# Kernel optimization log

Measured on AMD Instinct MI355X. Metric: run time of the kernel, lower is better.

Reference implementation:

```python
import jax, jax.numpy as jnp
import numpy as np

N_NODES = 100000
N_EDGES = 3200000  # avg degree 32
D_IN = 128
D_OUT = 64
BN_EPS = 0.001


def setup_inputs() -> dict:
    key = jax.random.key(0)
    k1, k2, k3, k4, k5 = jax.random.split(key, 5)
    x = jax.random.normal(k1, (N_NODES, D_IN), dtype=jnp.float32)
    W = jax.random.normal(k2, (D_IN, D_OUT), dtype=jnp.float32) * 0.05
    edge_val = jax.random.uniform(k3, (N_EDGES,), dtype=jnp.float32)
    edge_src = jax.random.randint(k4, (N_EDGES,), 0, N_NODES, dtype=jnp.int32)
    edge_dst = jax.random.randint(k5, (N_EDGES,), 0, N_NODES, dtype=jnp.int32)
    return {"x": x, "W": W, "edge_val": edge_val,
            "edge_src": edge_src, "edge_dst": edge_dst}


def reference(x, W, edge_val, edge_src, edge_dst):
    # pre_sup = X @ W  (dense feature transform; dropout rate is 0 -> identity)
    pre_sup = x @ W  # [N, D_OUT]
    # support = A @ pre_sup, A given in COO form: A[dst, src] = edge_val
    msgs = edge_val[:, None] * pre_sup[edge_src]          # [E, D_OUT]
    out = jax.ops.segment_sum(msgs, edge_dst, num_segments=N_NODES)  # [N, D_OUT]
    # tf.nn.moments over all-but-last axis + batch_norm (no scale/offset, eps=1e-3)
    mean = jnp.mean(out, axis=0)
    var = jnp.var(out, axis=0)
    out = (out - mean) * jax.lax.rsqrt(var + BN_EPS)
    return jax.nn.relu(out)
```

## Files before the change

kernel.cpp:

```cpp
#include <hip/hip_runtime.h>
#include <stdint.h>

#define D_IN  128
#define D_OUT 64
#define BN_EPS 1e-3f

#define BIN_SHIFT 6
#define BIN_NODES 64
#define BIN_CAP   2560
#define CHUNK     8192
#define MAX_BINS  1600
#define PT_STRIDE 72

typedef __attribute__((ext_vector_type(8))) short bf16x8;
typedef __attribute__((ext_vector_type(4))) float f32x4;

__device__ __forceinline__ ushort f32_to_bf16_rne(float f) {
  uint u = __float_as_uint(f);
  u += 0x7FFFu + ((u >> 16) & 1u);
  return (ushort)(u >> 16);
}
__device__ __forceinline__ float bf16_to_f32(ushort h) {
  return __uint_as_float((uint)h << 16);
}

__global__ __launch_bounds__(256) void gemm_mfma_kernel(
    const float* __restrict__ x, const float* __restrict__ W,
    ushort* __restrict__ pre16, int* __restrict__ bin_cursor,
    float* __restrict__ stats, int n_bins, int n_nodes, int n_tiles) {
  __shared__ ushort Wb[D_IN * D_OUT];
  __shared__ ushort ptile[64 * PT_STRIDE];
  const int t = threadIdx.x;
  if (blockIdx.x == 0) {
    for (int i = t; i < n_bins; i += 256) bin_cursor[i] = 0;
    if (t < 128) stats[t] = 0.f;
  }
  for (int i = t; i < D_IN * D_OUT; i += 256) Wb[i] = f32_to_bf16_rne(W[i]);
  __syncthreads();

  const int lane = t & 63;
  const int wave = t >> 6;
  const int m = lane & 15;
  const int quad = lane >> 4;

  bf16x8 bfrag[4][4];
#pragma unroll
  for (int nt = 0; nt < 4; ++nt)
#pragma unroll
    for (int s = 0; s < 4; ++s)
#pragma unroll
      for (int j = 0; j < 8; ++j)
        bfrag[nt][s][j] =
            (short)Wb[(32 * s + quad * 8 + j) * D_OUT + nt * 16 + m];

  for (int tile = blockIdx.x; tile < n_tiles; tile += gridDim.x) {
    const int rbase0 = tile * 64;
    const int row = rbase0 + wave * 16 + m;
    const size_t rl = (size_t)min(row, n_nodes - 1);
    f32x4 acc0 = {0.f, 0.f, 0.f, 0.f}, acc1 = {0.f, 0.f, 0.f, 0.f};
    f32x4 acc2 = {0.f, 0.f, 0.f, 0.f}, acc3 = {0.f, 0.f, 0.f, 0.f};
#pragma unroll
    for (int s = 0; s < 4; ++s) {
      const float4 xa = *(const float4*)&x[rl * D_IN + s * 32 + quad * 8];
      const float4 xb = *(const float4*)&x[rl * D_IN + s * 32 + quad * 8 + 4];
      bf16x8 af;
      af[0] = (short)f32_to_bf16_rne(xa.x);
      af[1] = (short)f32_to_bf16_rne(xa.y);
      af[2] = (short)f32_to_bf16_rne(xa.z);
      af[3] = (short)f32_to_bf16_rne(xa.w);
      af[4] = (short)f32_to_bf16_rne(xb.x);
      af[5] = (short)f32_to_bf16_rne(xb.y);
      af[6] = (short)f32_to_bf16_rne(xb.z);
      af[7] = (short)f32_to_bf16_rne(xb.w);
      acc0 = __builtin_amdgcn_mfma_f32_16x16x32_bf16(af, bfrag[0][s], acc0, 0, 0, 0);
      acc1 = __builtin_amdgcn_mfma_f32_16x16x32_bf16(af, bfrag[1][s], acc1, 0, 0, 0);
      acc2 = __builtin_amdgcn_mfma_f32_16x16x32_bf16(af, bfrag[2][s], acc2, 0, 0, 0);
      acc3 = __builtin_amdgcn_mfma_f32_16x16x32_bf16(af, bfrag[3][s], acc3, 0, 0, 0);
    }
    __syncthreads();
#pragma unroll
    for (int reg = 0; reg < 4; ++reg) {
      const int lr = wave * 16 + quad * 4 + reg;
      ptile[lr * PT_STRIDE + m]      = f32_to_bf16_rne(acc0[reg]);
      ptile[lr * PT_STRIDE + 16 + m] = f32_to_bf16_rne(acc1[reg]);
      ptile[lr * PT_STRIDE + 32 + m] = f32_to_bf16_rne(acc2[reg]);
      ptile[lr * PT_STRIDE + 48 + m] = f32_to_bf16_rne(acc3[reg]);
    }
    __syncthreads();
    {
      const int lr = t >> 2;
      const int sg = t & 3;
      const int r = rbase0 + lr;
      if (r < n_nodes) {
        const uint4* pl = (const uint4*)&ptile[lr * PT_STRIDE + sg * 16];
        uint4* po = (uint4*)&pre16[(size_t)r * D_OUT + sg * 16];
        po[0] = pl[0];
        po[1] = pl[1];
      }
    }
  }
}

__global__ __launch_bounds__(256) void partition_kernel(
    const float* __restrict__ ev, const int* __restrict__ esrc,
    const int* __restrict__ edst, int* __restrict__ bin_cursor,
    uint2* __restrict__ bucket, int n_edges, int n_bins) {
  __shared__ int cnt[MAX_BINS];
  __shared__ int base[MAX_BINS];
  const int t = threadIdx.x;
  const int beg = blockIdx.x * CHUNK;
  const int end = min(beg + CHUNK, n_edges);

  for (int i = t; i < n_bins; i += 256) cnt[i] = 0;
  __syncthreads();

  for (int i = beg + t * 4; i < end; i += 1024) {
    if (i + 3 < end) {
      const int4 d4 = *(const int4*)&edst[i];
      atomicAdd(&cnt[d4.x >> BIN_SHIFT], 1);
      atomicAdd(&cnt[d4.y >> BIN_SHIFT], 1);
      atomicAdd(&cnt[d4.z >> BIN_SHIFT], 1);
      atomicAdd(&cnt[d4.w >> BIN_SHIFT], 1);
    } else {
      for (int k = i; k < end; ++k) atomicAdd(&cnt[edst[k] >> BIN_SHIFT], 1);
    }
  }
  __syncthreads();

  for (int i = t; i < n_bins; i += 256) {
    const int c = cnt[i];
    int b = 0;
    if (c > 0) b = atomicAdd(&bin_cursor[i], c);
    if (b > BIN_CAP) b = BIN_CAP;
    base[i] = i * BIN_CAP + b;
    cnt[i] = 0;
  }
  __syncthreads();

  for (int i = beg + t * 4; i < end; i += 1024) {
    if (i + 3 < end) {
      const int4 d4 = *(const int4*)&edst[i];
      const int4 s4 = *(const int4*)&esrc[i];
      const float4 v4 = *(const float4*)&ev[i];
#pragma unroll
      for (int k = 0; k < 4; ++k) {
        const int dst = (&d4.x)[k];
        const int src = (&s4.x)[k];
        const float v = (&v4.x)[k];
        const int bin = dst >> BIN_SHIFT;
        const int r = atomicAdd(&cnt[bin], 1);
        const int pos = base[bin] + r;
        if (pos < (bin + 1) * BIN_CAP) {
          const uint w0 = ((uint)(dst & (BIN_NODES - 1)) << 17) | (uint)src;
          bucket[pos] = make_uint2(w0, __float_as_uint(v));
        }
      }
    } else {
      for (int k = i; k < end; ++k) {
        const int dst = edst[k];
        const int bin = dst >> BIN_SHIFT;
        const int r = atomicAdd(&cnt[bin], 1);
        const int pos = base[bin] + r;
        if (pos < (bin + 1) * BIN_CAP) {
          const uint w0 = ((uint)(dst & (BIN_NODES - 1)) << 17) | (uint)esrc[k];
          bucket[pos] = make_uint2(w0, __float_as_uint(ev[k]));
        }
      }
    }
  }
}

__global__ __launch_bounds__(512) void bin_sort_gather_kernel(
    const ushort* __restrict__ pre16, const uint2* __restrict__ bucket,
    const int* __restrict__ bin_cursor, float* __restrict__ out,
    float* __restrict__ stats, int n_nodes) {
  __shared__ uint s_src[BIN_CAP];
  __shared__ ushort s_val[BIN_CAP];
  __shared__ int s_hist[BIN_NODES];
  __shared__ int s_off[BIN_NODES + 1];
  __shared__ int s_cur[BIN_NODES];

  const int t = threadIdx.x;
  const int bin = blockIdx.x;
  const int cnt = min(bin_cursor[bin], BIN_CAP);
  const int64_t rbase = (int64_t)bin * BIN_CAP;

  if (t < BIN_NODES) s_hist[t] = 0;
  __syncthreads();

  for (int i = t; i < cnt; i += 512)
    atomicAdd(&s_hist[bucket[rbase + i].x >> 17], 1);
  __syncthreads();

  int own = (t < BIN_NODES) ? s_hist[t] : 0;
  for (int off = 1; off < BIN_NODES; off <<= 1) {
    int u = 0;
    if (t < BIN_NODES && t >= off) u = s_hist[t - off];
    __syncthreads();
    if (t < BIN_NODES) s_hist[t] += u;
    __syncthreads();
  }
  if (t < BIN_NODES) {
    const int e = s_hist[t] - own;
    s_off[t] = e;
    s_cur[t] = e;
  }
  if (t == 0) s_off[BIN_NODES] = cnt;
  __syncthreads();

  for (int i = t; i < cnt; i += 512) {
    const uint2 r = bucket[rbase + i];
    const int d = r.x >> 17;
    const int p = atomicAdd(&s_cur[d], 1);
    s_src[p] = r.x & 0x1FFFFu;
    s_val[p] = f32_to_bf16_rne(__uint_as_float(r.y));
  }
  __syncthreads();

  const int lane = t & 63;
  const int wave = t >> 6;
  const int half = lane >> 5;
  const int hl = lane & 31;
  const int node0 = bin * BIN_NODES;
  float csx = 0.f, csy = 0.f, cs2x = 0.f, cs2y = 0.f;

  for (int nl = wave; nl < BIN_NODES; nl += 8) {
    const int node = node0 + nl;
    if (node < n_nodes) {
      const int jb = s_off[nl], je = s_off[nl + 1];
      float a0x = 0.f, a0y = 0.f, a1x = 0.f, a1y = 0.f;
      float a2x = 0.f, a2y = 0.f, a3x = 0.f, a3y = 0.f;
      float a4x = 0.f, a4y = 0.f, a5x = 0.f, a5y = 0.f;
      float a6x = 0.f, a6y = 0.f, a7x = 0.f, a7y = 0.f;
      int j = jb + half;
      for (; j + 14 < je; j += 16) {
        const uint src0 = s_src[j],      src1 = s_src[j + 2];
        const uint src2 = s_src[j + 4],  src3 = s_src[j + 6];
        const uint src4 = s_src[j + 8],  src5 = s_src[j + 10];
        const uint src6 = s_src[j + 12], src7 = s_src[j + 14];
        const float v0 = bf16_to_f32(s_val[j]);
        const float v1 = bf16_to_f32(s_val[j + 2]);
        const float v2 = bf16_to_f32(s_val[j + 4]);
        const float v3 = bf16_to_f32(s_val[j + 6]);
        const float v4 = bf16_to_f32(s_val[j + 8]);
        const float v5 = bf16_to_f32(s_val[j + 10]);
        const float v6 = bf16_to_f32(s_val[j + 12]);
        const float v7 = bf16_to_f32(s_val[j + 14]);
        const uint p0 = *(const uint*)&pre16[(size_t)src0 * D_OUT + 2 * hl];
        const uint p1 = *(const uint*)&pre16[(size_t)src1 * D_OUT + 2 * hl];
        const uint p2 = *(const uint*)&pre16[(size_t)src2 * D_OUT + 2 * hl];
        const uint p3 = *(const uint*)&pre16[(size_t)src3 * D_OUT + 2 * hl];
        const uint p4 = *(const uint*)&pre16[(size_t)src4 * D_OUT + 2 * hl];
        const uint p5 = *(const uint*)&pre16[(size_t)src5 * D_OUT + 2 * hl];
        const uint p6 = *(const uint*)&pre16[(size_t)src6 * D_OUT + 2 * hl];
        const uint p7 = *(const uint*)&pre16[(size_t)src7 * D_OUT + 2 * hl];
        a0x += v0 * bf16_to_f32((ushort)(p0 & 0xFFFFu));
        a0y += v0 * bf16_to_f32((ushort)(p0 >> 16));
        a1x += v1 * bf16_to_f32((ushort)(p1 & 0xFFFFu));
        a1y += v1 * bf16_to_f32((ushort)(p1 >> 16));
        a2x += v2 * bf16_to_f32((ushort)(p2 & 0xFFFFu));
        a2y += v2 * bf16_to_f32((ushort)(p2 >> 16));
        a3x += v3 * bf16_to_f32((ushort)(p3 & 0xFFFFu));
        a3y += v3 * bf16_to_f32((ushort)(p3 >> 16));
        a4x += v4 * bf16_to_f32((ushort)(p4 & 0xFFFFu));
        a4y += v4 * bf16_to_f32((ushort)(p4 >> 16));
        a5x += v5 * bf16_to_f32((ushort)(p5 & 0xFFFFu));
        a5y += v5 * bf16_to_f32((ushort)(p5 >> 16));
        a6x += v6 * bf16_to_f32((ushort)(p6 & 0xFFFFu));
        a6y += v6 * bf16_to_f32((ushort)(p6 >> 16));
        a7x += v7 * bf16_to_f32((ushort)(p7 & 0xFFFFu));
        a7y += v7 * bf16_to_f32((ushort)(p7 >> 16));
      }
      for (; j + 6 < je; j += 8) {
        const uint src0 = s_src[j],     src1 = s_src[j + 2];
        const uint src2 = s_src[j + 4], src3 = s_src[j + 6];
        const float v0 = bf16_to_f32(s_val[j]);
        const float v1 = bf16_to_f32(s_val[j + 2]);
        const float v2 = bf16_to_f32(s_val[j + 4]);
        const float v3 = bf16_to_f32(s_val[j + 6]);
        const uint p0 = *(const uint*)&pre16[(size_t)src0 * D_OUT + 2 * hl];
        const uint p1 = *(const uint*)&pre16[(size_t)src1 * D_OUT + 2 * hl];
        const uint p2 = *(const uint*)&pre16[(size_t)src2 * D_OUT + 2 * hl];
        const uint p3 = *(const uint*)&pre16[(size_t)src3 * D_OUT + 2 * hl];
        a0x += v0 * bf16_to_f32((ushort)(p0 & 0xFFFFu));
        a0y += v0 * bf16_to_f32((ushort)(p0 >> 16));
        a1x += v1 * bf16_to_f32((ushort)(p1 & 0xFFFFu));
        a1y += v1 * bf16_to_f32((ushort)(p1 >> 16));
        a2x += v2 * bf16_to_f32((ushort)(p2 & 0xFFFFu));
        a2y += v2 * bf16_to_f32((ushort)(p2 >> 16));
        a3x += v3 * bf16_to_f32((ushort)(p3 & 0xFFFFu));
        a3y += v3 * bf16_to_f32((ushort)(p3 >> 16));
      }
      for (; j < je; j += 2) {
        const uint src = s_src[j];
        const float v = bf16_to_f32(s_val[j]);
        const uint p = *(const uint*)&pre16[(size_t)src * D_OUT + 2 * hl];
        a0x += v * bf16_to_f32((ushort)(p & 0xFFFFu));
        a0y += v * bf16_to_f32((ushort)(p >> 16));
      }
      float ax = ((a0x + a1x) + (a2x + a3x)) + ((a4x + a5x) + (a6x + a7x));
      float ay = ((a0y + a1y) + (a2y + a3y)) + ((a4y + a5y) + (a6y + a7y));
      ax += __shfl_xor(ax, 32);
      ay += __shfl_xor(ay, 32);
      if (half == 0) {
        *(float2*)&out[(size_t)node * D_OUT + 2 * hl] = make_float2(ax, ay);
        csx += ax;
        cs2x += ax * ax;
        csy += ay;
        cs2y += ay * ay;
      }
    }
  }
  __syncthreads();

  float* red = (float*)s_src;
  float* red2 = red + 512;
  if (half == 0) {
    red[wave * 64 + 2 * hl] = csx;
    red[wave * 64 + 2 * hl + 1] = csy;
    red2[wave * 64 + 2 * hl] = cs2x;
    red2[wave * 64 + 2 * hl + 1] = cs2y;
  }
  __syncthreads();
  if (t < 64) {
    float s = 0.f, s2 = 0.f;
#pragma unroll
    for (int wv = 0; wv < 8; ++wv) {
      s += red[wv * 64 + t];
      s2 += red2[wv * 64 + t];
    }
    atomicAdd(&stats[t], s);
    atomicAdd(&stats[64 + t], s2);
  }
}

__global__ __launch_bounds__(256) void norm_kernel(
    float* __restrict__ out, const float* __restrict__ stats, int64_t n_vec4,
    float inv_n) {
  const int c = (threadIdx.x * 4) & 63;
  float mean[4], scale[4];
#pragma unroll
  for (int k = 0; k < 4; ++k) {
    mean[k] = stats[c + k] * inv_n;
    const float var = stats[64 + c + k] * inv_n - mean[k] * mean[k];
    scale[k] = rsqrtf(var + BN_EPS);
  }
  const int64_t stride = (int64_t)gridDim.x * 256;
  for (int64_t i = (int64_t)blockIdx.x * 256 + threadIdx.x; i < n_vec4;
       i += stride) {
    float4 v = ((float4*)out)[i];
    v.x = (v.x - mean[0]) * scale[0];
    v.y = (v.y - mean[1]) * scale[1];
    v.z = (v.z - mean[2]) * scale[2];
    v.w = (v.w - mean[3]) * scale[3];
    v.x = v.x > 0.f ? v.x : 0.f;
    v.y = v.y > 0.f ? v.y : 0.f;
    v.z = v.z > 0.f ? v.z : 0.f;
    v.w = v.w > 0.f ? v.w : 0.f;
    ((float4*)out)[i] = v;
  }
}

extern "C" void kernel_launch(void* const* d_in, const int* in_sizes, int n_in,
                              void* d_out, int out_size, void* d_ws,
                              size_t ws_size, hipStream_t stream) {
  const float* x = (const float*)d_in[0];
  const float* W = (const float*)d_in[1];
  const float* ev = (const float*)d_in[2];
  const int* esrc = (const int*)d_in[3];
  const int* edst = (const int*)d_in[4];

  const int n_nodes = in_sizes[0] / D_IN;
  const int n_edges = in_sizes[2];
  const int64_t n_out = (int64_t)n_nodes * D_OUT;
  const int n_bins = (n_nodes + BIN_NODES - 1) >> BIN_SHIFT;
  const int n_row_tiles = (n_nodes + 63) / 64;

  float* out = (float*)d_out;

  char* w = (char*)d_ws;
  ushort* pre16 = (ushort*)w;             w += (size_t)n_nodes * D_OUT * 2;
  int* bin_cursor = (int*)w;              w += (size_t)n_bins * 4;
  float* stats = (float*)w;               w += 128 * 4;
  w = (char*)(((uintptr_t)w + 7) & ~(uintptr_t)7);
  uint2* bucket = (uint2*)w;

  gemm_mfma_kernel<<<(n_row_tiles + 1) / 2, 256, 0, stream>>>(
      x, W, pre16, bin_cursor, stats, n_bins, n_nodes, n_row_tiles);
  partition_kernel<<<(n_edges + CHUNK - 1) / CHUNK, 256, 0, stream>>>(
      ev, esrc, edst, bin_cursor, bucket, n_edges, n_bins);
  bin_sort_gather_kernel<<<n_bins, 512, 0, stream>>>(pre16, bucket, bin_cursor,
                                                     out, stats, n_nodes);
  norm_kernel<<<2048, 256, 0, stream>>>(out, stats, n_out / 4,
                                        1.0f / (float)n_nodes);
}
```

Baseline: 299.3 us.

## Merge GEMM and edge partition into one launch with role-split blocks

Combines the dense MFMA GEMM and the edge-binning partition kernel into a single launch, where the first n_gemm blocks do the feature transform and the remaining blocks partition edges. The two independent phases can then run concurrently on the GPU and one launch gap disappears. Zeroing of the bin cursors and stats moves from GEMM block 0 into a hipMemsetAsync, which removes the ordering dependency that would otherwise make partitioning race with the reset. The shared memory becomes a union sized for the larger role, and the memset adds a small extra stream operation.

```diff
diff --git a/kernel.cpp b/kernel.cpp
--- a/kernel.cpp
+++ b/kernel.cpp
@@ -24,146 +24,143 @@
   return __uint_as_float((uint)h << 16);
 }
 
-__global__ __launch_bounds__(256) void gemm_mfma_kernel(
+__global__ __launch_bounds__(256) void gemm_partition_kernel(
     const float* __restrict__ x, const float* __restrict__ W,
-    ushort* __restrict__ pre16, int* __restrict__ bin_cursor,
-    float* __restrict__ stats, int n_bins, int n_nodes, int n_tiles) {
-  __shared__ ushort Wb[D_IN * D_OUT];
-  __shared__ ushort ptile[64 * PT_STRIDE];
+    const float* __restrict__ ev, const int* __restrict__ esrc,
+    const int* __restrict__ edst, ushort* __restrict__ pre16,
+    int* __restrict__ bin_cursor, uint2* __restrict__ bucket,
+    int n_nodes, int n_tiles, int n_edges, int n_bins, int n_gemm) {
+  __shared__ char smem[25600];
   const int t = threadIdx.x;
-  if (blockIdx.x == 0) {
-    for (int i = t; i < n_bins; i += 256) bin_cursor[i] = 0;
-    if (t < 128) stats[t] = 0.f;
-  }
-  for (int i = t; i < D_IN * D_OUT; i += 256) Wb[i] = f32_to_bf16_rne(W[i]);
-  __syncthreads();
-
-  const int lane = t & 63;
-  const int wave = t >> 6;
-  const int m = lane & 15;
-  const int quad = lane >> 4;
-
-  bf16x8 bfrag[4][4];
-#pragma unroll
-  for (int nt = 0; nt < 4; ++nt)
-#pragma unroll
-    for (int s = 0; s < 4; ++s)
-#pragma unroll
-      for (int j = 0; j < 8; ++j)
-        bfrag[nt][s][j] =
-            (short)Wb[(32 * s + quad * 8 + j) * D_OUT + nt * 16 + m];
-
-  for (int tile = blockIdx.x; tile < n_tiles; tile += gridDim.x) {
-    const int rbase0 = tile * 64;
-    const int row = rbase0 + wave * 16 + m;
-    const size_t rl = (size_t)min(row, n_nodes - 1);
-    f32x4 acc0 = {0.f, 0.f, 0.f, 0.f}, acc1 = {0.f, 0.f, 0.f, 0.f};
-    f32x4 acc2 = {0.f, 0.f, 0.f, 0.f}, acc3 = {0.f, 0.f, 0.f, 0.f};
-#pragma unroll
-    for (int s = 0; s < 4; ++s) {
-      const float4 xa = *(const float4*)&x[rl * D_IN + s * 32 + quad * 8];
-      const float4 xb = *(const float4*)&x[rl * D_IN + s * 32 + quad * 8 + 4];
-      bf16x8 af;
-      af[0] = (short)f32_to_bf16_rne(xa.x);
-      af[1] = (short)f32_to_bf16_rne(xa.y);
-      af[2] = (short)f32_to_bf16_rne(xa.z);
-      af[3] = (short)f32_to_bf16_rne(xa.w);
-      af[4] = (short)f32_to_bf16_rne(xb.x);
-      af[5] = (short)f32_to_bf16_rne(xb.y);
-      af[6] = (short)f32_to_bf16_rne(xb.z);
-      af[7] = (short)f32_to_bf16_rne(xb.w);
-      acc0 = __builtin_amdgcn_mfma_f32_16x16x32_bf16(af, bfrag[0][s], acc0, 0, 0, 0);
-      acc1 = __builtin_amdgcn_mfma_f32_16x16x32_bf16(af, bfrag[1][s], acc1, 0, 0, 0);
-      acc2 = __builtin_amdgcn_mfma_f32_16x16x32_bf16(af, bfrag[2][s], acc2, 0, 0, 0);
-      acc3 = __builtin_amdgcn_mfma_f32_16x16x32_bf16(af, bfrag[3][s], acc3, 0, 0, 0);
-    }
-    __syncthreads();
-#pragma unroll
-    for (int reg = 0; reg < 4; ++reg) {
-      const int lr = wave * 16 + quad * 4 + reg;
-      ptile[lr * PT_STRIDE + m]      = f32_to_bf16_rne(acc0[reg]);
-      ptile[lr * PT_STRIDE + 16 + m] = f32_to_bf16_rne(acc1[reg]);
-      ptile[lr * PT_STRIDE + 32 + m] = f32_to_bf16_rne(acc2[reg]);
-      ptile[lr * PT_STRIDE + 48 + m] = f32_to_bf16_rne(acc3[reg]);
-    }
-    __syncthreads();
-    {
-      const int lr = t >> 2;
-      const int sg = t & 3;
-      const int r = rbase0 + lr;
-      if (r < n_nodes) {
-        const uint4* pl = (const uint4*)&ptile[lr * PT_STRIDE + sg * 16];
-        uint4* po = (uint4*)&pre16[(size_t)r * D_OUT + sg * 16];
-        po[0] = pl[0];
-        po[1] = pl[1];
-      }
-    }
-  }
-}
-
-__global__ __launch_bounds__(256) void partition_kernel(
-    const float* __restrict__ ev, const int* __restrict__ esrc,
-    const int* __restrict__ edst, int* __restrict__ bin_cursor,
-    uint2* __restrict__ bucket, int n_edges, int n_bins) {
-  __shared__ int cnt[MAX_BINS];
-  __shared__ int base[MAX_BINS];
-  const int t = threadIdx.x;
-  const int beg = blockIdx.x * CHUNK;
-  const int end = min(beg + CHUNK, n_edges);
-
-  for (int i = t; i < n_bins; i += 256) cnt[i] = 0;
-  __syncthreads();
-
-  for (int i = beg + t * 4; i < end; i += 1024) {
-    if (i + 3 < end) {
-      const int4 d4 = *(const int4*)&edst[i];
-      atomicAdd(&cnt[d4.x >> BIN_SHIFT], 1);
-      atomicAdd(&cnt[d4.y >> BIN_SHIFT], 1);
-      atomicAdd(&cnt[d4.z >> BIN_SHIFT], 1);
-      atomicAdd(&cnt[d4.w >> BIN_SHIFT], 1);
-    } else {
-      for (int k = i; k < end; ++k) atomicAdd(&cnt[edst[k] >> BIN_SHIFT], 1);
-    }
-  }
-  __syncthreads();
-
-  for (int i = t; i < n_bins; i += 256) {
-    const int c = cnt[i];
-    int b = 0;
-    if (c > 0) b = atomicAdd(&bin_cursor[i], c);
-    if (b > BIN_CAP) b = BIN_CAP;
-    base[i] = i * BIN_CAP + b;
-    cnt[i] = 0;
-  }
-  __syncthreads();
-
-  for (int i = beg + t * 4; i < end; i += 1024) {
-    if (i + 3 < end) {
-      const int4 d4 = *(const int4*)&edst[i];
-      const int4 s4 = *(const int4*)&esrc[i];
-      const float4 v4 = *(const float4*)&ev[i];
-#pragma unroll
-      for (int k = 0; k < 4; ++k) {
-        const int dst = (&d4.x)[k];
-        const int src = (&s4.x)[k];
-        const float v = (&v4.x)[k];
-        const int bin = dst >> BIN_SHIFT;
-        const int r = atomicAdd(&cnt[bin], 1);
-        const int pos = base[bin] + r;
-        if (pos < (bin + 1) * BIN_CAP) {
-          const uint w0 = ((uint)(dst & (BIN_NODES - 1)) << 17) | (uint)src;
-          bucket[pos] = make_uint2(w0, __float_as_uint(v));
+
+  if ((int)blockIdx.x < n_gemm) {
+    ushort* Wb = (ushort*)smem;
+    ushort* ptile = (ushort*)(smem + 16384);
+    for (int i = t; i < D_IN * D_OUT; i += 256) Wb[i] = f32_to_bf16_rne(W[i]);
+    __syncthreads();
+
+    const int lane = t & 63;
+    const int wave = t >> 6;
+    const int m = lane & 15;
+    const int quad = lane >> 4;
+
+    bf16x8 bfrag[4][4];
+#pragma unroll
+    for (int nt = 0; nt < 4; ++nt)
+#pragma unroll
+      for (int s = 0; s < 4; ++s)
+#pragma unroll
+        for (int j = 0; j < 8; ++j)
+          bfrag[nt][s][j] =
+              (short)Wb[(32 * s + quad * 8 + j) * D_OUT + nt * 16 + m];
+
+    for (int tile = blockIdx.x; tile < n_tiles; tile += n_gemm) {
+      const int rbase0 = tile * 64;
+      const int row = rbase0 + wave * 16 + m;
+      const size_t rl = (size_t)min(row, n_nodes - 1);
+      f32x4 acc0 = {0.f, 0.f, 0.f, 0.f}, acc1 = {0.f, 0.f, 0.f, 0.f};
+      f32x4 acc2 = {0.f, 0.f, 0.f, 0.f}, acc3 = {0.f, 0.f, 0.f, 0.f};
+#pragma unroll
+      for (int s = 0; s < 4; ++s) {
+        const float4 xa = *(const float4*)&x[rl * D_IN + s * 32 + quad * 8];
+        const float4 xb = *(const float4*)&x[rl * D_IN + s * 32 + quad * 8 + 4];
+        bf16x8 af;
+        af[0] = (short)f32_to_bf16_rne(xa.x);
+        af[1] = (short)f32_to_bf16_rne(xa.y);
+        af[2] = (short)f32_to_bf16_rne(xa.z);
+        af[3] = (short)f32_to_bf16_rne(xa.w);
+        af[4] = (short)f32_to_bf16_rne(xb.x);
+        af[5] = (short)f32_to_bf16_rne(xb.y);
+        af[6] = (short)f32_to_bf16_rne(xb.z);
+        af[7] = (short)f32_to_bf16_rne(xb.w);
+        acc0 = __builtin_amdgcn_mfma_f32_16x16x32_bf16(af, bfrag[0][s], acc0, 0, 0, 0);
+        acc1 = __builtin_amdgcn_mfma_f32_16x16x32_bf16(af, bfrag[1][s], acc1, 0, 0, 0);
+        acc2 = __builtin_amdgcn_mfma_f32_16x16x32_bf16(af, bfrag[2][s], acc2, 0, 0, 0);
+        acc3 = __builtin_amdgcn_mfma_f32_16x16x32_bf16(af, bfrag[3][s], acc3, 0, 0, 0);
+      }
+      __syncthreads();
+#pragma unroll
+      for (int reg = 0; reg < 4; ++reg) {
+        const int lr = wave * 16 + quad * 4 + reg;
+        ptile[lr * PT_STRIDE + m]      = f32_to_bf16_rne(acc0[reg]);
+        ptile[lr * PT_STRIDE + 16 + m] = f32_to_bf16_rne(acc1[reg]);
+        ptile[lr * PT_STRIDE + 32 + m] = f32_to_bf16_rne(acc2[reg]);
+        ptile[lr * PT_STRIDE + 48 + m] = f32_to_bf16_rne(acc3[reg]);
+      }
+      __syncthreads();
+      {
+        const int lr = t >> 2;
+        const int sg = t & 3;
+        const int r = rbase0 + lr;
+        if (r < n_nodes) {
+          const uint4* pl = (const uint4*)&ptile[lr * PT_STRIDE + sg * 16];
+          uint4* po = (uint4*)&pre16[(size_t)r * D_OUT + sg * 16];
+          po[0] = pl[0];
+          po[1] = pl[1];
         }
       }
-    } else {
-      for (int k = i; k < end; ++k) {
-        const int dst = edst[k];
-        const int bin = dst >> BIN_SHIFT;
-        const int r = atomicAdd(&cnt[bin], 1);
-        const int pos = base[bin] + r;
-        if (pos < (bin + 1) * BIN_CAP) {
-          const uint w0 = ((uint)(dst & (BIN_NODES - 1)) << 17) | (uint)esrc[k];
-          bucket[pos] = make_uint2(w0, __float_as_uint(ev[k]));
+    }
+  } else {
+    int* cnt = (int*)smem;
+    int* base = (int*)(smem + MAX_BINS * 4);
+    const int bp = (int)blockIdx.x - n_gemm;
+    const int beg = bp * CHUNK;
+    const int end = min(beg + CHUNK, n_edges);
+
+    for (int i = t; i < n_bins; i += 256) cnt[i] = 0;
+    __syncthreads();
+
+    for (int i = beg + t * 4; i < end; i += 1024) {
+      if (i + 3 < end) {
+        const int4 d4 = *(const int4*)&edst[i];
+        atomicAdd(&cnt[d4.x >> BIN_SHIFT], 1);
+        atomicAdd(&cnt[d4.y >> BIN_SHIFT], 1);
+        atomicAdd(&cnt[d4.z >> BIN_SHIFT], 1);
+        atomicAdd(&cnt[d4.w >> BIN_SHIFT], 1);
+      } else {
+        for (int k = i; k < end; ++k) atomicAdd(&cnt[edst[k] >> BIN_SHIFT], 1);
+      }
+    }
+    __syncthreads();
+
+    for (int i = t; i < n_bins; i += 256) {
+      const int c = cnt[i];
+      int b = 0;
+      if (c > 0) b = atomicAdd(&bin_cursor[i], c);
+      if (b > BIN_CAP) b = BIN_CAP;
+      base[i] = i * BIN_CAP + b;
+      cnt[i] = 0;
+    }
+    __syncthreads();
+
+    for (int i = beg + t * 4; i < end; i += 1024) {
+      if (i + 3 < end) {
+        const int4 d4 = *(const int4*)&edst[i];
+        const int4 s4 = *(const int4*)&esrc[i];
+        const float4 v4 = *(const float4*)&ev[i];
+#pragma unroll
+        for (int k = 0; k < 4; ++k) {
+          const int dst = (&d4.x)[k];
+          const int src = (&s4.x)[k];
+          const float v = (&v4.x)[k];
+          const int bin = dst >> BIN_SHIFT;
+          const int r = atomicAdd(&cnt[bin], 1);
+          const int pos = base[bin] + r;
+          if (pos < (bin + 1) * BIN_CAP) {
+            const uint w0 = ((uint)(dst & (BIN_NODES - 1)) << 17) | (uint)src;
+            bucket[pos] = make_uint2(w0, __float_as_uint(v));
+          }
+        }
+      } else {
+        for (int k = i; k < end; ++k) {
+          const int dst = edst[k];
+          const int bin = dst >> BIN_SHIFT;
+          const int r = atomicAdd(&cnt[bin], 1);
+          const int pos = base[bin] + r;
+          if (pos < (bin + 1) * BIN_CAP) {
+            const uint w0 = ((uint)(dst & (BIN_NODES - 1)) << 17) | (uint)esrc[k];
+            bucket[pos] = make_uint2(w0, __float_as_uint(ev[k]));
+          }
         }
       }
     }
@@ -375,6 +372,8 @@
   const int64_t n_out = (int64_t)n_nodes * D_OUT;
   const int n_bins = (n_nodes + BIN_NODES - 1) >> BIN_SHIFT;
   const int n_row_tiles = (n_nodes + 63) / 64;
+  const int n_gemm = (n_row_tiles + 1) / 2;
+  const int n_part = (n_edges + CHUNK - 1) / CHUNK;
 
   float* out = (float*)d_out;
 
@@ -385,10 +384,10 @@
   w = (char*)(((uintptr_t)w + 7) & ~(uintptr_t)7);
   uint2* bucket = (uint2*)w;
 
-  gemm_mfma_kernel<<<(n_row_tiles + 1) / 2, 256, 0, stream>>>(
-      x, W, pre16, bin_cursor, stats, n_bins, n_nodes, n_row_tiles);
-  partition_kernel<<<(n_edges + CHUNK - 1) / CHUNK, 256, 0, stream>>>(
-      ev, esrc, edst, bin_cursor, bucket, n_edges, n_bins);
+  hipMemsetAsync(bin_cursor, 0, (size_t)n_bins * 4 + 128 * 4, stream);
+  gemm_partition_kernel<<<n_gemm + n_part, 256, 0, stream>>>(
+      x, W, ev, esrc, edst, pre16, bin_cursor, bucket, n_nodes, n_row_tiles,
+      n_edges, n_bins, n_gemm);
   bin_sort_gather_kernel<<<n_bins, 512, 0, stream>>>(pre16, bucket, bin_cursor,
                                                      out, stats, n_nodes);
   norm_kernel<<<2048, 256, 0, stream>>>(out, stats, n_out / 4,
```

Result: no change. 298.9 us (-0.1%).
